# Kernel optimization log

Hardware: AMD Instinct MI355X
Metric: run time of the kernel (lower is better)

The kernel has to match this reference:

```python
import jax, jax.numpy as jnp
import numpy as np

N_NODES = 50000
N_EDGES = 800000
IN_DIM = 128
HIDDEN = 128
HEADS = 2
C = HIDDEN // HEADS  # per-head channels
N_CLASSES = 32
N_GRAPHS = 64
NEG_SLOPE = 0.2  # PyG GATConv default negative_slope


def setup_inputs() -> dict:
    key = jax.random.key(0)
    ks = jax.random.split(key, 16)
    x = jax.random.normal(ks[0], (N_NODES, IN_DIM), dtype=jnp.float32)
    edge_index = jax.random.randint(ks[1], (2, N_EDGES), 0, N_NODES, dtype=jnp.int64)
    batch = jnp.sort(jax.random.randint(ks[2], (N_NODES,), 0, N_GRAPHS, dtype=jnp.int64))
    s_in = 1.0 / np.sqrt(IN_DIM)
    s_h = 1.0 / np.sqrt(HIDDEN)
    s_c = 1.0 / np.sqrt(C)
    W1 = jax.random.normal(ks[3], (HEADS * C, IN_DIM), jnp.float32) * s_in
    att_src1 = jax.random.normal(ks[4], (HEADS, C), jnp.float32) * s_c
    att_dst1 = jax.random.normal(ks[5], (HEADS, C), jnp.float32) * s_c
    b1 = jnp.zeros((HEADS * C,), jnp.float32)
    W2 = jax.random.normal(ks[6], (HEADS * C, HIDDEN), jnp.float32) * s_h
    att_src2 = jax.random.normal(ks[7], (HEADS, C), jnp.float32) * s_c
    att_dst2 = jax.random.normal(ks[8], (HEADS, C), jnp.float32) * s_c
    b2 = jnp.zeros((HEADS * C,), jnp.float32)
    fc_w = jax.random.normal(ks[9], (N_CLASSES, HIDDEN), jnp.float32) * s_h
    fc_b = jnp.zeros((N_CLASSES,), jnp.float32)
    return {"x": x, "edge_index": edge_index, "batch": batch,
            "W1": W1, "att_src1": att_src1, "att_dst1": att_dst1, "b1": b1,
            "W2": W2, "att_src2": att_src2, "att_dst2": att_dst2, "b2": b2,
            "fc_w": fc_w, "fc_b": fc_b}


def gat_conv(x, edge_index, W, att_src, att_dst, bias):
    """PyG GATConv (concat=True, add_self_loops=True, negative_slope=0.2)."""
    N = x.shape[0]
    loops = jnp.arange(N, dtype=edge_index.dtype)
    src = jnp.concatenate([edge_index[0], loops])  # [E+N]
    dst = jnp.concatenate([edge_index[1], loops])
    xl = (x @ W.T).reshape(N, HEADS, C)  # [N,H,C]
    a_src = jnp.einsum('nhc,hc->nh', xl, att_src)  # [N,H]
    a_dst = jnp.einsum('nhc,hc->nh', xl, att_dst)
    alpha = jax.nn.leaky_relu(a_src[src] + a_dst[dst], NEG_SLOPE)  # [E+N,H]
    # segment softmax over incoming edges of each dst node
    amax = jax.ops.segment_max(alpha, dst, num_segments=N)
    amax = jnp.where(jnp.isfinite(amax), amax, 0.0)
    ex = jnp.exp(alpha - amax[dst])
    denom = jax.ops.segment_sum(ex, dst, num_segments=N)
    coeff = ex / jnp.maximum(denom[dst], 1e-16)  # [E+N,H]
    msg = xl[src] * coeff[:, :, None]  # [E+N,H,C]
    out = jax.ops.segment_sum(msg, dst, num_segments=N)  # [N,H,C]
    return out.reshape(N, HEADS * C) + bias


def reference(x, edge_index, batch, W1, att_src1, att_dst1, b1,
              W2, att_src2, att_dst2, b2, fc_w, fc_b):
    h = jax.nn.relu(gat_conv(x, edge_index, W1, att_src1, att_dst1, b1))
    h = jax.nn.relu(gat_conv(h, edge_index, W2, att_src2, att_dst2, b2))
    # global_mean_pool over graphs
    sums = jax.ops.segment_sum(h, batch, num_segments=N_GRAPHS)  # [G,HIDDEN]
    counts = jax.ops.segment_sum(jnp.ones((h.shape[0],), h.dtype), batch, num_segments=N_GRAPHS)
    pooled = sums / jnp.maximum(counts, 1.0)[:, None]
    return pooled @ fc_w.T + fc_b  # [G, N_CLASSES]
```

## Files before the change

### kernel.cpp

```cpp
#include <hip/hip_runtime.h>
#include <hip/hip_bf16.h>


#define NEG_SLOPE 0.2f

typedef short bf16x8 __attribute__((ext_vector_type(8)));
typedef float f32x4 __attribute__((ext_vector_type(4)));

__device__ __forceinline__ float lrelu(float x) { return x > 0.f ? x : NEG_SLOPE * x; }
__device__ __forceinline__ float bf2f(unsigned short u) { return __uint_as_float(((unsigned)u) << 16); }
__device__ __forceinline__ unsigned short f2bf(float f) {
    unsigned x = __float_as_uint(f);
    return (unsigned short)((x + 0x7fffu + ((x >> 16) & 1u)) >> 16);
}

__global__ __launch_bounds__(256) void bucket_hist(const int* __restrict__ ei, int* __restrict__ bcount, int E) {
    __shared__ int hist[256];
    int t = threadIdx.x;
    hist[t] = 0;
    __syncthreads();
    int eb = blockIdx.x * 4096;
#pragma unroll
    for (int i = 0; i < 16; ++i) {
        int e = eb + i * 256 + t;
        if (e < E) atomicAdd(&hist[ei[E + e] >> 8], 1);
    }
    __syncthreads();
    if (hist[t]) atomicAdd(&bcount[t], hist[t]);
}

__global__ __launch_bounds__(256) void bucket_scan(const int* __restrict__ bcount, int* __restrict__ ebase,
                                                   int* __restrict__ bcur, int* __restrict__ offs, int NB, int N, int E) {
    __shared__ int sc[256];
    int t = threadIdx.x;
    int cnt = (t < NB) ? bcount[t] : 0;
    sc[t] = cnt;
    __syncthreads();
    for (int off = 1; off < 256; off <<= 1) {
        int x = (t >= off) ? sc[t - off] : 0;
        __syncthreads();
        sc[t] += x;
        __syncthreads();
    }
    int excl = sc[t] - cnt;
    if (t < NB) {
        ebase[t] = excl;
        bcur[t] = excl;
    }
    if (t == NB - 1) ebase[NB] = sc[t];
    if (t == 0) offs[N] = E + N;
}

__global__ __launch_bounds__(1024) void bucket_scatter(const int* __restrict__ ei, int* __restrict__ bcur,
                                                       unsigned* __restrict__ pk, int E) {
    __shared__ int hist[256];
    __shared__ int base[256];
    int t = threadIdx.x;
    if (t < 256) hist[t] = 0;
    __syncthreads();
    int eb = blockIdx.x * 16384;
    int d[16];
#pragma unroll
    for (int i = 0; i < 16; ++i) {
        int e = eb + i * 1024 + t;
        if (e < E) {
            d[i] = ei[E + e];
            atomicAdd(&hist[d[i] >> 8], 1);
        } else {
            d[i] = -1;
        }
    }
    __syncthreads();
    if (t < 256) {
        int c = hist[t];
        base[t] = c ? atomicAdd(&bcur[t], c) : 0;
        hist[t] = 0;
    }
    __syncthreads();
#pragma unroll
    for (int i = 0; i < 16; ++i) {
        if (d[i] >= 0) {
            int s = ei[eb + i * 1024 + t];
            int bk = d[i] >> 8;
            int r = atomicAdd(&hist[bk], 1);
            pk[base[bk] + r] = ((unsigned)s << 8) | (unsigned)(d[i] & 255);
        }
    }
}

__global__ __launch_bounds__(256) void csr_build(const unsigned* __restrict__ pk, const int* __restrict__ ebase,
                                                 int* __restrict__ offs, int* __restrict__ ssrc, int N) {
    __shared__ int deg[256];
    __shared__ int curs[256];
    __shared__ int sc[256];
    int t = threadIdx.x;
    int b = blockIdx.x;
    deg[t] = 0;
    __syncthreads();
    int e0 = ebase[b], e1 = ebase[b + 1];
    for (int j = e0 + t; j < e1; j += 256) atomicAdd(&deg[pk[j] & 255], 1);
    __syncthreads();
    int nb0 = b * 256;
    int ncount = min(256, N - nb0);
    int v = (t < ncount) ? deg[t] + 1 : 0;
    sc[t] = v;
    __syncthreads();
    for (int off = 1; off < 256; off <<= 1) {
        int x = (t >= off) ? sc[t - off] : 0;
        __syncthreads();
        sc[t] += x;
        __syncthreads();
    }
    int nbase = e0 + b * 256;
    if (t < ncount) {
        int o = nbase + sc[t] - v;
        offs[nb0 + t] = o;
        ssrc[o] = nb0 + t;
        curs[t] = o + 1;
    }
    __syncthreads();
    for (int j = e0 + t; j < e1; j += 256) {
        unsigned e = pk[j];
        int pos = atomicAdd(&curs[e & 255], 1);
        ssrc[pos] = (int)(e >> 8);
    }
}

__global__ void w_convert(const float* __restrict__ W1, const float* __restrict__ W2,
                          unsigned short* __restrict__ Wb1, unsigned short* __restrict__ Wb2) {
    int i = blockIdx.x * 256 + threadIdx.x;
    if (i < 16384) Wb1[i] = f2bf(W1[i]);
    else if (i < 32768) Wb2[i - 16384] = f2bf(W2[i - 16384]);
}

#define LDW 136
template <typename T>
__global__ __launch_bounds__(256) void gemm_kernel(const T* __restrict__ A, const unsigned short* __restrict__ Wb,
                                                   unsigned short* __restrict__ out,
                                                   const float* __restrict__ att_s, const float* __restrict__ att_d,
                                                   float* __restrict__ a_src, float* __restrict__ a_dst, int M) {
    __shared__ unsigned short Ws[128 * LDW];
    __shared__ unsigned short As[64 * LDW];
    int tid = threadIdx.x;
    int m0 = blockIdx.x * 64;
#pragma unroll
    for (int i = 0; i < 8; ++i) {
        int slot = i * 256 + tid;
        int r = slot >> 4;
        int c8 = (slot & 15) << 3;
        uint4 u = *(const uint4*)(Wb + r * 128 + c8);
        *(uint4*)(&Ws[r * LDW + c8]) = u;
    }
    if constexpr (sizeof(T) == 4) {
#pragma unroll
        for (int i = 0; i < 8; ++i) {
            int slot = i * 256 + tid;
            int r = slot >> 5;
            int c4 = (slot & 31) << 2;
            int m = m0 + r;
            float4 v = make_float4(0.f, 0.f, 0.f, 0.f);
            if (m < M) v = *(const float4*)((const float*)A + (size_t)m * 128 + c4);
            ushort4 w4;
            w4.x = f2bf(v.x); w4.y = f2bf(v.y); w4.z = f2bf(v.z); w4.w = f2bf(v.w);
            *(ushort4*)(&As[r * LDW + c4]) = w4;
        }
    } else {
#pragma unroll
        for (int i = 0; i < 4; ++i) {
            int slot = i * 256 + tid;
            int r = slot >> 4;
            int c8 = (slot & 15) << 3;
            int m = m0 + r;
            uint4 u = make_uint4(0, 0, 0, 0);
            if (m < M) u = *(const uint4*)((const unsigned short*)A + (size_t)m * 128 + c8);
            *(uint4*)(&As[r * LDW + c8]) = u;
        }
    }
    __syncthreads();
    int w = tid >> 6, l = tid & 63;
    int lr = l & 15;
    int lk = (l >> 4) << 3;
    f32x4 acc0 = {0.f, 0.f, 0.f, 0.f}, acc1 = acc0, acc2 = acc0, acc3 = acc0;
    f32x4 acc4 = acc0, acc5 = acc0, acc6 = acc0, acc7 = acc0;
    int arow = (w * 16 + lr) * LDW;
#pragma unroll
    for (int ks = 0; ks < 4; ++ks) {
        int kb = ks * 32 + lk;
        bf16x8 af = *(const bf16x8*)(&As[arow + kb]);
#define MSTEP(i) { bf16x8 bfv = *(const bf16x8*)(&Ws[((i) * 16 + lr) * LDW + kb]); \
                   acc##i = __builtin_amdgcn_mfma_f32_16x16x32_bf16(af, bfv, acc##i, 0, 0, 0); }
        MSTEP(0) MSTEP(1) MSTEP(2) MSTEP(3) MSTEP(4) MSTEP(5) MSTEP(6) MSTEP(7)
#undef MSTEP
    }
    int rbase = m0 + w * 16 + ((l >> 4) << 2);
#pragma unroll
    for (int j = 0; j < 4; ++j) {
        int m = rbase + j;
        if (m < M) {
            unsigned ob = (unsigned)m * 128 + (unsigned)lr;
            out[ob + 0]   = f2bf(acc0[j]);
            out[ob + 16]  = f2bf(acc1[j]);
            out[ob + 32]  = f2bf(acc2[j]);
            out[ob + 48]  = f2bf(acc3[j]);
            out[ob + 64]  = f2bf(acc4[j]);
            out[ob + 80]  = f2bf(acc5[j]);
            out[ob + 96]  = f2bf(acc6[j]);
            out[ob + 112] = f2bf(acc7[j]);
        }
    }
    float as0 = att_s[lr], as1 = att_s[16 + lr], as2 = att_s[32 + lr], as3 = att_s[48 + lr];
    float as4 = att_s[64 + lr], as5 = att_s[80 + lr], as6 = att_s[96 + lr], as7 = att_s[112 + lr];
    float ad0 = att_d[lr], ad1 = att_d[16 + lr], ad2 = att_d[32 + lr], ad3 = att_d[48 + lr];
    float ad4 = att_d[64 + lr], ad5 = att_d[80 + lr], ad6 = att_d[96 + lr], ad7 = att_d[112 + lr];
#pragma unroll
    for (int j = 0; j < 4; ++j) {
        float ps0 = acc0[j] * as0 + acc1[j] * as1 + acc2[j] * as2 + acc3[j] * as3;
        float pd0 = acc0[j] * ad0 + acc1[j] * ad1 + acc2[j] * ad2 + acc3[j] * ad3;
        float ps1 = acc4[j] * as4 + acc5[j] * as5 + acc6[j] * as6 + acc7[j] * as7;
        float pd1 = acc4[j] * ad4 + acc5[j] * ad5 + acc6[j] * ad6 + acc7[j] * ad7;
#pragma unroll
        for (int off = 1; off < 16; off <<= 1) {
            ps0 += __shfl_xor(ps0, off);
            pd0 += __shfl_xor(pd0, off);
            ps1 += __shfl_xor(ps1, off);
            pd1 += __shfl_xor(pd1, off);
        }
        if (lr == 0) {
            int m = rbase + j;
            if (m < M) {
                a_src[m * 2 + 0] = ps0;
                a_dst[m * 2 + 0] = pd0;
                a_src[m * 2 + 1] = ps1;
                a_dst[m * 2 + 1] = pd1;
            }
        }
    }
}

#define MAXD 128
__global__ __launch_bounds__(256) void gat_node_kernel(const unsigned short* __restrict__ XLb,
                                                       const float* __restrict__ a_src, const float* __restrict__ a_dst,
                                                       const int* __restrict__ offs, const int* __restrict__ ssrc,
                                                       const float* __restrict__ bias,
                                                       unsigned short* __restrict__ out, int N) {
    __shared__ float coeff[4][2][MAXD];
    __shared__ int srcs[4][MAXD];
    int t = threadIdx.x;
    int w = t >> 6, l = t & 63;
    int n = blockIdx.x * 4 + w;
    if (n >= N) return;
    int h = l >> 5, sl = l & 31;
    int c = 2 * l;
    int j0 = offs[n], j1 = offs[n + 1];
    int deg = j1 - j0;
    float ad = a_dst[n * 2 + h];
    float acc0 = 0.f, acc1 = 0.f;
    if (deg <= MAXD) {
        float m = -1e30f;
        for (int k = sl; k < deg; k += 32) {
            int s = ssrc[j0 + k];
            if (h == 0) srcs[w][k] = s;
            float al = lrelu(a_src[s * 2 + h] + ad);
            coeff[w][h][k] = al;
            m = fmaxf(m, al);
        }
#pragma unroll
        for (int off = 16; off > 0; off >>= 1) m = fmaxf(m, __shfl_xor(m, off));
        float sum = 0.f;
        for (int k = sl; k < deg; k += 32) {
            float e = __expf(coeff[w][h][k] - m);
            coeff[w][h][k] = e;
            sum += e;
        }
#pragma unroll
        for (int off = 16; off > 0; off >>= 1) sum += __shfl_xor(sum, off);
        float inv = 1.f / fmaxf(sum, 1e-16f);
        int j = 0;
        for (; j + 1 < deg; j += 2) {
            float c0 = coeff[w][h][j] * inv;
            float c1 = coeff[w][h][j + 1] * inv;
            unsigned s0 = (unsigned)srcs[w][j];
            unsigned s1 = (unsigned)srcs[w][j + 1];
            unsigned u0 = *(const unsigned*)(XLb + (s0 << 7) + c);
            unsigned u1 = *(const unsigned*)(XLb + (s1 << 7) + c);
            acc0 += c0 * __uint_as_float(u0 << 16) + c1 * __uint_as_float(u1 << 16);
            acc1 += c0 * __uint_as_float(u0 & 0xffff0000u) + c1 * __uint_as_float(u1 & 0xffff0000u);
        }
        if (j < deg) {
            float c0 = coeff[w][h][j] * inv;
            unsigned s0 = (unsigned)srcs[w][j];
            unsigned u0 = *(const unsigned*)(XLb + (s0 << 7) + c);
            acc0 += c0 * __uint_as_float(u0 << 16);
            acc1 += c0 * __uint_as_float(u0 & 0xffff0000u);
        }
    } else {
        float m = -1e30f;
        for (int k = sl; k < deg; k += 32) {
            int s = ssrc[j0 + k];
            m = fmaxf(m, lrelu(a_src[s * 2 + h] + ad));
        }
#pragma unroll
        for (int off = 16; off > 0; off >>= 1) m = fmaxf(m, __shfl_xor(m, off));
        float sum = 0.f;
        for (int k = sl; k < deg; k += 32) {
            int s = ssrc[j0 + k];
            sum += __expf(lrelu(a_src[s * 2 + h] + ad) - m);
        }
#pragma unroll
        for (int off = 16; off > 0; off >>= 1) sum += __shfl_xor(sum, off);
        float inv = 1.f / fmaxf(sum, 1e-16f);
        for (int j = 0; j < deg; ++j) {
            unsigned s = (unsigned)ssrc[j0 + j];
            float cc = __expf(lrelu(a_src[s * 2 + h] + ad) - m) * inv;
            unsigned u0 = *(const unsigned*)(XLb + (s << 7) + c);
            acc0 += cc * __uint_as_float(u0 << 16);
            acc1 += cc * __uint_as_float(u0 & 0xffff0000u);
        }
    }
    float o0 = fmaxf(acc0 + bias[c], 0.f);
    float o1 = fmaxf(acc1 + bias[c + 1], 0.f);
    *(unsigned*)(out + ((unsigned)n << 7) + c) = (unsigned)f2bf(o0) | ((unsigned)f2bf(o1) << 16);
}

#define PB 128
__global__ __launch_bounds__(128) void pool_kernel(const unsigned short* __restrict__ Hb,
                                                   const int* __restrict__ batch,
                                                   float* __restrict__ pooled, int* __restrict__ counts, int N) {
    __shared__ unsigned short Hs[PB * 128];
    __shared__ int bs[PB];
    int t = threadIdx.x;
    int base = blockIdx.x * PB;
    int lim = min(PB, N - base);
#pragma unroll
    for (int i = 0; i < 16; ++i) {
        int slot = i * 128 + t;
        int r = slot >> 4;
        int c8 = (slot & 15) << 3;
        uint4 u = make_uint4(0, 0, 0, 0);
        int n0 = base + r;
        if (n0 < N) u = *(const uint4*)(Hb + (size_t)n0 * 128 + c8);
        *(uint4*)(&Hs[r * 128 + c8]) = u;
    }
    if (t < lim) bs[t] = batch[base + t];
    __syncthreads();
    float acc = 0.f;
    int cur = bs[0];
    int runstart = 0;
    for (int i = 0; i < lim; ++i) {
        int g = bs[i];
        if (g != cur) {
            atomicAdd(&pooled[cur * 128 + t], acc);
            if (t == 0) atomicAdd(&counts[cur], i - runstart);
            cur = g;
            acc = 0.f;
            runstart = i;
        }
        acc += bf2f(Hs[i * 128 + t]);
    }
    atomicAdd(&pooled[cur * 128 + t], acc);
    if (t == 0) atomicAdd(&counts[cur], lim - runstart);
}

__global__ void final_kernel(const float* __restrict__ pooled, const int* __restrict__ counts,
                             const float* __restrict__ fc_w, const float* __restrict__ fc_b,
                             float* __restrict__ out) {
    int idx = blockIdx.x * 256 + threadIdx.x;
    if (idx >= 64 * 32) return;
    int g = idx >> 5, k = idx & 31;
    float invc = 1.f / fmaxf((float)counts[g], 1.f);
    float s = 0.f;
#pragma unroll 4
    for (int c = 0; c < 128; ++c) s += pooled[g * 128 + c] * fc_w[k * 128 + c];
    out[idx] = s * invc + fc_b[k];
}

extern "C" void kernel_launch(void* const* d_in, const int* in_sizes, int n_in,
                              void* d_out, int out_size, void* d_ws, size_t ws_size,
                              hipStream_t stream) {
    const float* x = (const float*)d_in[0];
    const int* ei = (const int*)d_in[1];
    const int* batch = (const int*)d_in[2];
    const float* W1 = (const float*)d_in[3];
    const float* as1 = (const float*)d_in[4];
    const float* ad1 = (const float*)d_in[5];
    const float* b1 = (const float*)d_in[6];
    const float* W2 = (const float*)d_in[7];
    const float* as2 = (const float*)d_in[8];
    const float* ad2 = (const float*)d_in[9];
    const float* b2 = (const float*)d_in[10];
    const float* fcw = (const float*)d_in[11];
    const float* fcb = (const float*)d_in[12];
    float* out = (float*)d_out;

    const int N = in_sizes[0] / 128;
    const int E = in_sizes[1] / 2;
    const int EN = E + N;
    const int NB = (N + 255) >> 8;

    char* p = (char*)d_ws;
    auto alloc = [&](size_t bytes) -> char* {
        char* r = p;
        p += (bytes + 255) & ~(size_t)255;
        return r;
    };
    unsigned short* XLb = (unsigned short*)alloc((size_t)N * 128 * 2);
    unsigned short* Hb = (unsigned short*)alloc((size_t)N * 128 * 2);
    float* a_src = (float*)alloc((size_t)N * 2 * 4);
    float* a_dst = (float*)alloc((size_t)N * 2 * 4);
    int* offs = (int*)alloc((size_t)(N + 1) * 4);
    int* ssrc = (int*)alloc((size_t)EN * 4);
    unsigned* pk = (unsigned*)alloc((size_t)E * 4);
    int* ebase = (int*)alloc((size_t)(NB + 1) * 4);
    int* bcur = (int*)alloc((size_t)NB * 4);
    unsigned short* Wb1 = (unsigned short*)alloc(16384 * 2);
    unsigned short* Wb2 = (unsigned short*)alloc(16384 * 2);
    float* pooled = (float*)alloc((8192 + 64 + 256) * 4);
    int* counts = (int*)(pooled + 8192);
    int* bcount = (int*)(pooled + 8192 + 64);

    const int TB = 256;
    int gGemm = (N + 63) / 64;
    int gWave = (N + 3) / 4;

    hipMemsetAsync(pooled, 0, (8192 + 64 + 256) * 4, stream);
    w_convert<<<128, TB, 0, stream>>>(W1, W2, Wb1, Wb2);

    bucket_hist<<<(E + 4095) / 4096, TB, 0, stream>>>(ei, bcount, E);
    bucket_scan<<<1, TB, 0, stream>>>(bcount, ebase, bcur, offs, NB, N, E);
    bucket_scatter<<<(E + 16383) / 16384, 1024, 0, stream>>>(ei, bcur, pk, E);
    csr_build<<<NB, TB, 0, stream>>>(pk, ebase, offs, ssrc, N);

    gemm_kernel<float><<<gGemm, TB, 0, stream>>>(x, Wb1, XLb, as1, ad1, a_src, a_dst, N);
    gat_node_kernel<<<gWave, TB, 0, stream>>>(XLb, a_src, a_dst, offs, ssrc, b1, Hb, N);

    gemm_kernel<unsigned short><<<gGemm, TB, 0, stream>>>(Hb, Wb2, XLb, as2, ad2, a_src, a_dst, N);
    gat_node_kernel<<<gWave, TB, 0, stream>>>(XLb, a_src, a_dst, offs, ssrc, b2, Hb, N);

    pool_kernel<<<(N + PB - 1) / PB, 128, 0, stream>>>(Hb, batch, pooled, counts, N);
    final_kernel<<<8, TB, 0, stream>>>(pooled, counts, fcw, fcb, out);
}
```

Baseline: 276.8 us.

## Fuse CSR build into cooperative kernel, enlarge GEMM tile, unroll aggregation

Merges the four CSR-construction kernels into a single cooperative kernel that uses grid-wide syncs, and folds the memset into the weight-conversion kernel, cutting launch count. The GEMM tile grows from 64 to 128 rows per block so each B fragment feeds two MFMAs. The node aggregation loop is unrolled by four, with softmax normalisation applied once at the end. The cooperative grid of 256 blocks does less parallel work per phase and adds grid.sync overhead.

```diff
diff --git a/kernel.cpp b/kernel.cpp
--- a/kernel.cpp
+++ b/kernel.cpp
@@ -1,5 +1,8 @@
 #include <hip/hip_runtime.h>
 #include <hip/hip_bf16.h>
+#include <hip/hip_cooperative_groups.h>
+
+namespace cg = cooperative_groups;
 
 
 #define NEG_SLOPE 0.2f
@@ -14,123 +17,118 @@
     return (unsigned short)((x + 0x7fffu + ((x >> 16) & 1u)) >> 16);
 }
 
-__global__ __launch_bounds__(256) void bucket_hist(const int* __restrict__ ei, int* __restrict__ bcount, int E) {
-    __shared__ int hist[256];
-    int t = threadIdx.x;
-    hist[t] = 0;
-    __syncthreads();
-    int eb = blockIdx.x * 4096;
-#pragma unroll
-    for (int i = 0; i < 16; ++i) {
-        int e = eb + i * 256 + t;
-        if (e < E) atomicAdd(&hist[ei[E + e] >> 8], 1);
-    }
-    __syncthreads();
-    if (hist[t]) atomicAdd(&bcount[t], hist[t]);
-}
-
-__global__ __launch_bounds__(256) void bucket_scan(const int* __restrict__ bcount, int* __restrict__ ebase,
-                                                   int* __restrict__ bcur, int* __restrict__ offs, int NB, int N, int E) {
-    __shared__ int sc[256];
-    int t = threadIdx.x;
-    int cnt = (t < NB) ? bcount[t] : 0;
-    sc[t] = cnt;
-    __syncthreads();
-    for (int off = 1; off < 256; off <<= 1) {
-        int x = (t >= off) ? sc[t - off] : 0;
-        __syncthreads();
-        sc[t] += x;
-        __syncthreads();
-    }
-    int excl = sc[t] - cnt;
-    if (t < NB) {
-        ebase[t] = excl;
-        bcur[t] = excl;
-    }
-    if (t == NB - 1) ebase[NB] = sc[t];
-    if (t == 0) offs[N] = E + N;
-}
-
-__global__ __launch_bounds__(1024) void bucket_scatter(const int* __restrict__ ei, int* __restrict__ bcur,
-                                                       unsigned* __restrict__ pk, int E) {
-    __shared__ int hist[256];
-    __shared__ int base[256];
-    int t = threadIdx.x;
-    if (t < 256) hist[t] = 0;
-    __syncthreads();
-    int eb = blockIdx.x * 16384;
-    int d[16];
-#pragma unroll
-    for (int i = 0; i < 16; ++i) {
-        int e = eb + i * 1024 + t;
-        if (e < E) {
-            d[i] = ei[E + e];
-            atomicAdd(&hist[d[i] >> 8], 1);
-        } else {
-            d[i] = -1;
-        }
-    }
-    __syncthreads();
-    if (t < 256) {
-        int c = hist[t];
-        base[t] = c ? atomicAdd(&bcur[t], c) : 0;
-        hist[t] = 0;
-    }
-    __syncthreads();
-#pragma unroll
-    for (int i = 0; i < 16; ++i) {
-        if (d[i] >= 0) {
-            int s = ei[eb + i * 1024 + t];
-            int bk = d[i] >> 8;
-            int r = atomicAdd(&hist[bk], 1);
-            pk[base[bk] + r] = ((unsigned)s << 8) | (unsigned)(d[i] & 255);
-        }
-    }
-}
-
-__global__ __launch_bounds__(256) void csr_build(const unsigned* __restrict__ pk, const int* __restrict__ ebase,
-                                                 int* __restrict__ offs, int* __restrict__ ssrc, int N) {
-    __shared__ int deg[256];
-    __shared__ int curs[256];
-    __shared__ int sc[256];
+__global__ __launch_bounds__(256) void csr_coop(const int* __restrict__ ei, int* __restrict__ bcount,
+                                                int* __restrict__ ebase, int* __restrict__ bcur,
+                                                int* __restrict__ offs, unsigned* __restrict__ pk,
+                                                int* __restrict__ ssrc, int N, int E, int NB) {
+    __shared__ int h1[256];
+    __shared__ int h2[256];
+    __shared__ int h3[256];
+    cg::grid_group grid = cg::this_grid();
     int t = threadIdx.x;
     int b = blockIdx.x;
-    deg[t] = 0;
+    int G = gridDim.x;
+
+    h1[t] = 0;
     __syncthreads();
-    int e0 = ebase[b], e1 = ebase[b + 1];
-    for (int j = e0 + t; j < e1; j += 256) atomicAdd(&deg[pk[j] & 255], 1);
+    for (int e = b * 256 + t; e < E; e += G * 256)
+        atomicAdd(&h1[ei[E + e] >> 8], 1);
     __syncthreads();
-    int nb0 = b * 256;
-    int ncount = min(256, N - nb0);
-    int v = (t < ncount) ? deg[t] + 1 : 0;
-    sc[t] = v;
-    __syncthreads();
-    for (int off = 1; off < 256; off <<= 1) {
-        int x = (t >= off) ? sc[t - off] : 0;
-        __syncthreads();
-        sc[t] += x;
-        __syncthreads();
-    }
-    int nbase = e0 + b * 256;
-    if (t < ncount) {
-        int o = nbase + sc[t] - v;
-        offs[nb0 + t] = o;
-        ssrc[o] = nb0 + t;
-        curs[t] = o + 1;
-    }
-    __syncthreads();
-    for (int j = e0 + t; j < e1; j += 256) {
-        unsigned e = pk[j];
-        int pos = atomicAdd(&curs[e & 255], 1);
-        ssrc[pos] = (int)(e >> 8);
+    if (h1[t]) atomicAdd(&bcount[t], h1[t]);
+    grid.sync();
+
+    if (b == 0) {
+        int cnt = (t < NB) ? bcount[t] : 0;
+        h1[t] = cnt;
+        __syncthreads();
+        for (int off = 1; off < 256; off <<= 1) {
+            int x = (t >= off) ? h1[t - off] : 0;
+            __syncthreads();
+            h1[t] += x;
+            __syncthreads();
+        }
+        int excl = h1[t] - cnt;
+        if (t < NB) {
+            ebase[t] = excl;
+            bcur[t] = excl;
+        }
+        if (t == NB - 1) ebase[NB] = h1[t];
+        if (t == 0) offs[N] = E + N;
+    }
+    grid.sync();
+
+    for (int eb = b * 4096; eb < E; eb += G * 4096) {
+        h1[t] = 0;
+        __syncthreads();
+        int d[16], s[16];
+#pragma unroll
+        for (int i = 0; i < 16; ++i) {
+            int e = eb + i * 256 + t;
+            if (e < E) {
+                d[i] = ei[E + e];
+                s[i] = ei[e];
+                atomicAdd(&h1[d[i] >> 8], 1);
+            } else {
+                d[i] = -1;
+            }
+        }
+        __syncthreads();
+        h2[t] = h1[t] ? atomicAdd(&bcur[t], h1[t]) : 0;
+        h1[t] = 0;
+        __syncthreads();
+#pragma unroll
+        for (int i = 0; i < 16; ++i) {
+            if (d[i] >= 0) {
+                int bk = d[i] >> 8;
+                int r = atomicAdd(&h1[bk], 1);
+                pk[h2[bk] + r] = ((unsigned)s[i] << 8) | (unsigned)(d[i] & 255);
+            }
+        }
+        __syncthreads();
+    }
+    grid.sync();
+
+    for (int bk = b; bk < NB; bk += G) {
+        h1[t] = 0;
+        __syncthreads();
+        int e0 = ebase[bk], e1 = ebase[bk + 1];
+        for (int j = e0 + t; j < e1; j += 256) atomicAdd(&h1[pk[j] & 255], 1);
+        __syncthreads();
+        int nb0 = bk * 256;
+        int ncount = min(256, N - nb0);
+        int v = (t < ncount) ? h1[t] + 1 : 0;
+        h2[t] = v;
+        __syncthreads();
+        for (int off = 1; off < 256; off <<= 1) {
+            int x = (t >= off) ? h2[t - off] : 0;
+            __syncthreads();
+            h2[t] += x;
+            __syncthreads();
+        }
+        int nbase = e0 + bk * 256;
+        if (t < ncount) {
+            int o = nbase + h2[t] - v;
+            offs[nb0 + t] = o;
+            ssrc[o] = nb0 + t;
+            h3[t] = o + 1;
+        }
+        __syncthreads();
+        for (int j = e0 + t; j < e1; j += 256) {
+            unsigned e = pk[j];
+            int pos = atomicAdd(&h3[e & 255], 1);
+            ssrc[pos] = (int)(e >> 8);
+        }
+        __syncthreads();
     }
 }
 
 __global__ void w_convert(const float* __restrict__ W1, const float* __restrict__ W2,
-                          unsigned short* __restrict__ Wb1, unsigned short* __restrict__ Wb2) {
+                          unsigned short* __restrict__ Wb1, unsigned short* __restrict__ Wb2,
+                          float* __restrict__ zbuf, int zn) {
     int i = blockIdx.x * 256 + threadIdx.x;
     if (i < 16384) Wb1[i] = f2bf(W1[i]);
     else if (i < 32768) Wb2[i - 16384] = f2bf(W2[i - 16384]);
+    if (i < zn) zbuf[i] = 0.f;
 }
 
 #define LDW 136
@@ -140,20 +138,19 @@
                                                    const float* __restrict__ att_s, const float* __restrict__ att_d,
                                                    float* __restrict__ a_src, float* __restrict__ a_dst, int M) {
     __shared__ unsigned short Ws[128 * LDW];
-    __shared__ unsigned short As[64 * LDW];
+    __shared__ unsigned short As[128 * LDW];
     int tid = threadIdx.x;
-    int m0 = blockIdx.x * 64;
+    int m0 = blockIdx.x * 128;
 #pragma unroll
     for (int i = 0; i < 8; ++i) {
         int slot = i * 256 + tid;
         int r = slot >> 4;
         int c8 = (slot & 15) << 3;
-        uint4 u = *(const uint4*)(Wb + r * 128 + c8);
-        *(uint4*)(&Ws[r * LDW + c8]) = u;
+        *(uint4*)(&Ws[r * LDW + c8]) = *(const uint4*)(Wb + r * 128 + c8);
     }
     if constexpr (sizeof(T) == 4) {
 #pragma unroll
-        for (int i = 0; i < 8; ++i) {
+        for (int i = 0; i < 16; ++i) {
             int slot = i * 256 + tid;
             int r = slot >> 5;
             int c4 = (slot & 31) << 2;
@@ -166,7 +163,7 @@
         }
     } else {
 #pragma unroll
-        for (int i = 0; i < 4; ++i) {
+        for (int i = 0; i < 8; ++i) {
             int slot = i * 256 + tid;
             int r = slot >> 4;
             int c8 = (slot & 15) << 3;
@@ -180,58 +177,62 @@
     int w = tid >> 6, l = tid & 63;
     int lr = l & 15;
     int lk = (l >> 4) << 3;
-    f32x4 acc0 = {0.f, 0.f, 0.f, 0.f}, acc1 = acc0, acc2 = acc0, acc3 = acc0;
-    f32x4 acc4 = acc0, acc5 = acc0, acc6 = acc0, acc7 = acc0;
-    int arow = (w * 16 + lr) * LDW;
+    f32x4 acc[2][8];
+#pragma unroll
+    for (int mt = 0; mt < 2; ++mt)
+#pragma unroll
+        for (int nt = 0; nt < 8; ++nt) acc[mt][nt] = (f32x4){0.f, 0.f, 0.f, 0.f};
 #pragma unroll
     for (int ks = 0; ks < 4; ++ks) {
         int kb = ks * 32 + lk;
-        bf16x8 af = *(const bf16x8*)(&As[arow + kb]);
-#define MSTEP(i) { bf16x8 bfv = *(const bf16x8*)(&Ws[((i) * 16 + lr) * LDW + kb]); \
-                   acc##i = __builtin_amdgcn_mfma_f32_16x16x32_bf16(af, bfv, acc##i, 0, 0, 0); }
-        MSTEP(0) MSTEP(1) MSTEP(2) MSTEP(3) MSTEP(4) MSTEP(5) MSTEP(6) MSTEP(7)
-#undef MSTEP
-    }
-    int rbase = m0 + w * 16 + ((l >> 4) << 2);
-#pragma unroll
-    for (int j = 0; j < 4; ++j) {
-        int m = rbase + j;
-        if (m < M) {
-            unsigned ob = (unsigned)m * 128 + (unsigned)lr;
-            out[ob + 0]   = f2bf(acc0[j]);
-            out[ob + 16]  = f2bf(acc1[j]);
-            out[ob + 32]  = f2bf(acc2[j]);
-            out[ob + 48]  = f2bf(acc3[j]);
-            out[ob + 64]  = f2bf(acc4[j]);
-            out[ob + 80]  = f2bf(acc5[j]);
-            out[ob + 96]  = f2bf(acc6[j]);
-            out[ob + 112] = f2bf(acc7[j]);
-        }
-    }
-    float as0 = att_s[lr], as1 = att_s[16 + lr], as2 = att_s[32 + lr], as3 = att_s[48 + lr];
-    float as4 = att_s[64 + lr], as5 = att_s[80 + lr], as6 = att_s[96 + lr], as7 = att_s[112 + lr];
-    float ad0 = att_d[lr], ad1 = att_d[16 + lr], ad2 = att_d[32 + lr], ad3 = att_d[48 + lr];
-    float ad4 = att_d[64 + lr], ad5 = att_d[80 + lr], ad6 = att_d[96 + lr], ad7 = att_d[112 + lr];
-#pragma unroll
-    for (int j = 0; j < 4; ++j) {
-        float ps0 = acc0[j] * as0 + acc1[j] * as1 + acc2[j] * as2 + acc3[j] * as3;
-        float pd0 = acc0[j] * ad0 + acc1[j] * ad1 + acc2[j] * ad2 + acc3[j] * ad3;
-        float ps1 = acc4[j] * as4 + acc5[j] * as5 + acc6[j] * as6 + acc7[j] * as7;
-        float pd1 = acc4[j] * ad4 + acc5[j] * ad5 + acc6[j] * ad6 + acc7[j] * ad7;
-#pragma unroll
-        for (int off = 1; off < 16; off <<= 1) {
-            ps0 += __shfl_xor(ps0, off);
-            pd0 += __shfl_xor(pd0, off);
-            ps1 += __shfl_xor(ps1, off);
-            pd1 += __shfl_xor(pd1, off);
-        }
-        if (lr == 0) {
+        bf16x8 af0 = *(const bf16x8*)(&As[(w * 32 + lr) * LDW + kb]);
+        bf16x8 af1 = *(const bf16x8*)(&As[(w * 32 + 16 + lr) * LDW + kb]);
+#pragma unroll
+        for (int nt = 0; nt < 8; ++nt) {
+            bf16x8 bf = *(const bf16x8*)(&Ws[(nt * 16 + lr) * LDW + kb]);
+            acc[0][nt] = __builtin_amdgcn_mfma_f32_16x16x32_bf16(af0, bf, acc[0][nt], 0, 0, 0);
+            acc[1][nt] = __builtin_amdgcn_mfma_f32_16x16x32_bf16(af1, bf, acc[1][nt], 0, 0, 0);
+        }
+    }
+    float asv[8], adv[8];
+#pragma unroll
+    for (int nt = 0; nt < 8; ++nt) {
+        asv[nt] = att_s[nt * 16 + lr];
+        adv[nt] = att_d[nt * 16 + lr];
+    }
+#pragma unroll
+    for (int mt = 0; mt < 2; ++mt) {
+        int rbase = m0 + w * 32 + mt * 16 + ((l >> 4) << 2);
+#pragma unroll
+        for (int j = 0; j < 4; ++j) {
             int m = rbase + j;
             if (m < M) {
-                a_src[m * 2 + 0] = ps0;
-                a_dst[m * 2 + 0] = pd0;
-                a_src[m * 2 + 1] = ps1;
-                a_dst[m * 2 + 1] = pd1;
+                unsigned ob = (unsigned)m * 128 + (unsigned)lr;
+#pragma unroll
+                for (int nt = 0; nt < 8; ++nt) out[ob + nt * 16] = f2bf(acc[mt][nt][j]);
+            }
+        }
+#pragma unroll
+        for (int j = 0; j < 4; ++j) {
+            float ps0 = acc[mt][0][j] * asv[0] + acc[mt][1][j] * asv[1] + acc[mt][2][j] * asv[2] + acc[mt][3][j] * asv[3];
+            float pd0 = acc[mt][0][j] * adv[0] + acc[mt][1][j] * adv[1] + acc[mt][2][j] * adv[2] + acc[mt][3][j] * adv[3];
+            float ps1 = acc[mt][4][j] * asv[4] + acc[mt][5][j] * asv[5] + acc[mt][6][j] * asv[6] + acc[mt][7][j] * asv[7];
+            float pd1 = acc[mt][4][j] * adv[4] + acc[mt][5][j] * adv[5] + acc[mt][6][j] * adv[6] + acc[mt][7][j] * adv[7];
+#pragma unroll
+            for (int off = 1; off < 16; off <<= 1) {
+                ps0 += __shfl_xor(ps0, off);
+                pd0 += __shfl_xor(pd0, off);
+                ps1 += __shfl_xor(ps1, off);
+                pd1 += __shfl_xor(pd1, off);
+            }
+            if (lr == 0) {
+                int m = rbase + j;
+                if (m < M) {
+                    a_src[m * 2 + 0] = ps0;
+                    a_dst[m * 2 + 0] = pd0;
+                    a_src[m * 2 + 1] = ps1;
+                    a_dst[m * 2 + 1] = pd1;
+                }
             }
         }
     }
@@ -276,23 +277,33 @@
         for (int off = 16; off > 0; off >>= 1) sum += __shfl_xor(sum, off);
         float inv = 1.f / fmaxf(sum, 1e-16f);
         int j = 0;
-        for (; j + 1 < deg; j += 2) {
-            float c0 = coeff[w][h][j] * inv;
-            float c1 = coeff[w][h][j + 1] * inv;
-            unsigned s0 = (unsigned)srcs[w][j];
+        for (; j + 3 < deg; j += 4) {
+            float c0 = coeff[w][h][j + 0];
+            float c1 = coeff[w][h][j + 1];
+            float c2 = coeff[w][h][j + 2];
+            float c3 = coeff[w][h][j + 3];
+            unsigned s0 = (unsigned)srcs[w][j + 0];
             unsigned s1 = (unsigned)srcs[w][j + 1];
+            unsigned s2 = (unsigned)srcs[w][j + 2];
+            unsigned s3 = (unsigned)srcs[w][j + 3];
             unsigned u0 = *(const unsigned*)(XLb + (s0 << 7) + c);
             unsigned u1 = *(const unsigned*)(XLb + (s1 << 7) + c);
-            acc0 += c0 * __uint_as_float(u0 << 16) + c1 * __uint_as_float(u1 << 16);
-            acc1 += c0 * __uint_as_float(u0 & 0xffff0000u) + c1 * __uint_as_float(u1 & 0xffff0000u);
-        }
-        if (j < deg) {
-            float c0 = coeff[w][h][j] * inv;
+            unsigned u2 = *(const unsigned*)(XLb + (s2 << 7) + c);
+            unsigned u3 = *(const unsigned*)(XLb + (s3 << 7) + c);
+            acc0 += c0 * __uint_as_float(u0 << 16) + c1 * __uint_as_float(u1 << 16)
+                  + c2 * __uint_as_float(u2 << 16) + c3 * __uint_as_float(u3 << 16);
+            acc1 += c0 * __uint_as_float(u0 & 0xffff0000u) + c1 * __uint_as_float(u1 & 0xffff0000u)
+                  + c2 * __uint_as_float(u2 & 0xffff0000u) + c3 * __uint_as_float(u3 & 0xffff0000u);
+        }
+        for (; j < deg; ++j) {
+            float c0 = coeff[w][h][j];
             unsigned s0 = (unsigned)srcs[w][j];
             unsigned u0 = *(const unsigned*)(XLb + (s0 << 7) + c);
             acc0 += c0 * __uint_as_float(u0 << 16);
             acc1 += c0 * __uint_as_float(u0 & 0xffff0000u);
         }
+        acc0 *= inv;
+        acc1 *= inv;
     } else {
         float m = -1e30f;
         for (int k = sl; k < deg; k += 32) {
@@ -392,10 +403,10 @@
     const float* fcb = (const float*)d_in[12];
     float* out = (float*)d_out;
 
-    const int N = in_sizes[0] / 128;
-    const int E = in_sizes[1] / 2;
+    int N = in_sizes[0] / 128;
+    int E = in_sizes[1] / 2;
     const int EN = E + N;
-    const int NB = (N + 255) >> 8;
+    int NB = (N + 255) >> 8;
 
     char* p = (char*)d_ws;
     auto alloc = [&](size_t bytes) -> char* {
@@ -417,18 +428,19 @@
     float* pooled = (float*)alloc((8192 + 64 + 256) * 4);
     int* counts = (int*)(pooled + 8192);
     int* bcount = (int*)(pooled + 8192 + 64);
+    int zn = 8192 + 64 + 256;
 
     const int TB = 256;
-    int gGemm = (N + 63) / 64;
+    int gGemm = (N + 127) / 128;
     int gWave = (N + 3) / 4;
 
-    hipMemsetAsync(pooled, 0, (8192 + 64 + 256) * 4, stream);
-    w_convert<<<128, TB, 0, stream>>>(W1, W2, Wb1, Wb2);
-
-    bucket_hist<<<(E + 4095) / 4096, TB, 0, stream>>>(ei, bcount, E);
-    bucket_scan<<<1, TB, 0, stream>>>(bcount, ebase, bcur, offs, NB, N, E);
-    bucket_scatter<<<(E + 16383) / 16384, 1024, 0, stream>>>(ei, bcur, pk, E);
-    csr_build<<<NB, TB, 0, stream>>>(pk, ebase, offs, ssrc, N);
+    w_convert<<<128, TB, 0, stream>>>(W1, W2, Wb1, Wb2, pooled, zn);
+
+    {
+        void* args[] = {(void*)&ei, (void*)&bcount, (void*)&ebase, (void*)&bcur,
+                        (void*)&offs, (void*)&pk, (void*)&ssrc, (void*)&N, (void*)&E, (void*)&NB};
+        hipLaunchCooperativeKernel(reinterpret_cast<void*>(csr_coop), dim3(256), dim3(TB), args, 0, stream);
+    }
 
     gemm_kernel<float><<<gGemm, TB, 0, stream>>>(x, Wb1, XLb, as1, ad1, a_src, a_dst, N);
     gat_node_kernel<<<gWave, TB, 0, stream>>>(XLb, a_src, a_dst, offs, ssrc, b1, Hb, N);
```

After: 363.7 us. +31.4%, slower.
